# Performance work log

Hardware: AMD Instinct MI355X
Metric: run time of the kernel (lower is better)

Reference implementation:

```python
import jax, jax.numpy as jnp
import numpy as np

# irreps_in = irreps_out = 64x0e + 32x1o
MUL0, MUL1 = 64, 32          # multiplicities of 0e scalars and 1o vectors
DIM_IN = MUL0 + MUL1 * 3     # 160
N_NODES = 50000
IU0, IV0 = np.triu_indices(MUL0, k=1)   # 2016 scalar u<v pairs
IU1, IV1 = np.triu_indices(MUL1, k=1)   # 496 vector u<v pairs
# e3nn path normalization (component / element):
#   i_out=0 (0e): num_elements sum = 2016 + 64 + 496 + 32 = 2608, dim(0e)=1
#   i_out=1 (1o): num_elements = 32*64 = 2048, dim(1o)=3
C0 = float(np.sqrt(1.0 / 2608.0))
C1 = float(np.sqrt(3.0 / 2048.0))
INV_SQRT3 = float(1.0 / np.sqrt(3.0))   # w3j(1,0,1) and w3j(1,1,0) CG factor


def setup_inputs() -> dict:
    key = jax.random.key(0)
    ks = jax.random.split(key, 7)
    node_feats = jax.random.normal(ks[0], (N_NODES, DIM_IN), jnp.float32)
    node_messages = jax.random.normal(ks[1], (N_NODES, DIM_IN), jnp.float32)
    W1 = jax.random.normal(ks[2], (len(IU0), MUL0), jnp.float32)  # (0e,0e)->0e u<vw
    W2 = jax.random.normal(ks[3], (MUL0, MUL0), jnp.float32)      # (0e,0e)->0e uuw
    W3 = jax.random.normal(ks[4], (MUL1, MUL0, MUL1), jnp.float32)  # (1o,0e)->1o uvw
    W4 = jax.random.normal(ks[5], (len(IU1), MUL0), jnp.float32)  # (1o,1o)->0e u<vw
    W5 = jax.random.normal(ks[6], (MUL1, MUL0), jnp.float32)      # (1o,1o)->0e uuw
    return {"node_feats": node_feats, "node_messages": node_messages,
            "W1": W1, "W2": W2, "W3": W3, "W4": W4, "W5": W5}


def _tensor_square(x, W1, W2, W3, W4, W5):
    x0 = x[:, :MUL0]                        # [N, 64] scalars (0e)
    x1 = x[:, MUL0:].reshape(-1, MUL1, 3)   # [N, 32, 3] vectors (1o)
    # (0e x 0e) -> 0e
    pair0 = x0[:, IU0] * x0[:, IV0]         # [N, 2016]
    sq0 = x0 * x0                           # [N, 64]
    # (1o x 1o) -> 0e via dot products (w3j(1,1,0) = delta/sqrt3)
    d = jnp.einsum('nui,nvi->nuv', x1, x1)  # [N, 32, 32]
    pair1 = d[:, IU1, IV1] * INV_SQRT3      # [N, 496]
    diag1 = jnp.einsum('nui,nui->nu', x1, x1) * INV_SQRT3  # [N, 32]
    out0 = C0 * (pair0 @ W1 + sq0 @ W2 + pair1 @ W4 + diag1 @ W5)  # [N, 64]
    # (1o x 0e) -> 1o fully connected uvw (w3j(1,0,1) = eye/sqrt3)
    out1 = (C1 * INV_SQRT3) * jnp.einsum('nui,nv,uvw->nwi', x1, x0, W3)  # [N,32,3]
    return jnp.concatenate([out0, out1.reshape(-1, MUL1 * 3)], axis=1)


def reference(node_feats, node_messages, W1, W2, W3, W4, W5):
    x = node_feats + node_messages
    return _tensor_square(x, W1, W2, W3, W4, W5)
```

## Files before the change

### kernel.cpp

```cpp
#include <hip/hip_runtime.h>

typedef unsigned short u16;
typedef unsigned int u32;

#define N_NODES 50000
#define NB      64

#define BG_OFF  0
#define BT_OFF  262144
#define BH_OFF  327680

#define ASTR   72
#define AHSTR  40
#define XTSTR  68

typedef __attribute__((ext_vector_type(8))) short short8;
typedef __attribute__((ext_vector_type(4))) float f32x4;
union U4S8 { uint4 u; short8 s; };

__device__ __forceinline__ u16 f2bf(float f) {
    u32 u = __float_as_uint(f);
    return (u16)((u + 0x7fffu + ((u >> 16) & 1u)) >> 16);
}

__global__ __launch_bounds__(256)
void pack_kernel(const float* __restrict__ W1, const float* __restrict__ W2,
                 const float* __restrict__ W3, const float* __restrict__ W4,
                 const float* __restrict__ W5, u16* __restrict__ ws) {
    const float INV_SQRT3 = 0.57735026918962576f;
    int T = blockIdx.x * 256 + threadIdx.x;
    float val;
    if (T < BT_OFF) {
        int slot = T;
        int ntile = slot >> 10, rem = slot & 1023;
        int ks = rem >> 9, rem2 = rem & 511;
        int lane = rem2 >> 3, jj = rem2 & 7;
        int v = ks * 32 + (lane >> 4) * 8 + jj;
        int j = ntile * 16 + (lane & 15);
        int u = j >> 6, w = j & 63;
        if (v == u) val = W2[v * 64 + w];
        else {
            int a = min(u, v), b = max(u, v);
            int p = a * (127 - a) / 2 + (b - a - 1);
            val = 0.5f * W1[p * 64 + w];
        }
    } else if (T < BH_OFF) {
        int slot = T - BT_OFF;
        int ntile = slot >> 10, rem = slot & 1023;
        int ks = rem >> 9, rem2 = rem & 511;
        int lane = rem2 >> 3, jj = rem2 & 7;
        int v = ks * 32 + (lane >> 4) * 8 + jj;
        int j = ntile * 16 + (lane & 15);
        int u = j >> 5, w = j & 31;
        val = W3[(u * 64 + v) * 32 + w];
    } else {
        int slot = T - BH_OFF;
        int ntile = slot >> 9, rem = slot & 511;
        int lane = rem >> 3, jj = rem & 7;
        int v = (lane >> 4) * 8 + jj;
        int j = ntile * 16 + (lane & 15);
        int u = j >> 6, w = j & 63;
        if (v == u) val = W5[v * 64 + w] * INV_SQRT3;
        else {
            int a = min(u, v), b = max(u, v);
            int p = a * (63 - a) / 2 + (b - a - 1);
            val = W4[p * 64 + w] * (0.5f * INV_SQRT3);
        }
    }
    ws[T] = f2bf(val);
}

__global__ __launch_bounds__(256)
void node_block_kernel(const float* __restrict__ feats, const float* __restrict__ msgs,
                       const u16* __restrict__ ws, float* __restrict__ out) {
    __shared__ u16  A_S[64 * ASTR];
    __shared__ u16  A_H[192 * AHSTR];
    __shared__ float x0T[64 * XTSTR];
    __shared__ float x1T[96 * XTSTR];

    const int tid = threadIdx.x;
    const int node0 = blockIdx.x * NB;

    for (int k = 0; k < 5; ++k) {
        int chunk = tid + k * 256;
        int idx = chunk * 8;
        int n = (u32)idx / 160u;
        int d = idx - n * 160;
        int g = node0 * 160 + idx;
        float v[8];
        if (g + 8 <= N_NODES * 160) {
            float4 fa0 = *(const float4*)(feats + g);
            float4 fa1 = *(const float4*)(feats + g + 4);
            float4 fb0 = *(const float4*)(msgs + g);
            float4 fb1 = *(const float4*)(msgs + g + 4);
            v[0]=fa0.x+fb0.x; v[1]=fa0.y+fb0.y; v[2]=fa0.z+fb0.z; v[3]=fa0.w+fb0.w;
            v[4]=fa1.x+fb1.x; v[5]=fa1.y+fb1.y; v[6]=fa1.z+fb1.z; v[7]=fa1.w+fb1.w;
        } else {
            #pragma unroll
            for (int j = 0; j < 8; ++j) v[j] = 0.f;
        }
        if (d < 64) {
            uint4 pk;
            pk.x = ((u32)f2bf(v[1]) << 16) | f2bf(v[0]);
            pk.y = ((u32)f2bf(v[3]) << 16) | f2bf(v[2]);
            pk.z = ((u32)f2bf(v[5]) << 16) | f2bf(v[4]);
            pk.w = ((u32)f2bf(v[7]) << 16) | f2bf(v[6]);
            *(uint4*)&A_S[n * ASTR + d] = pk;
            #pragma unroll
            for (int j = 0; j < 8; ++j) x0T[(d + j) * XTSTR + n] = v[j];
        } else {
            #pragma unroll
            for (int j = 0; j < 8; ++j) {
                int dd = d + j - 64;
                int u = (u32)dd / 3u, i = dd - u * 3;
                A_H[(i * 64 + n) * AHSTR + u] = f2bf(v[j]);
                x1T[(u * 3 + i) * XTSTR + n] = v[j];
            }
        }
    }
    __syncthreads();

    const int wave = tid >> 6, lane = tid & 63, quad = lane >> 4, l15 = lane & 15;
    const int wq = wave;
    const f32x4 z4 = {0.f, 0.f, 0.f, 0.f};

    f32x4 o0[4];
    #pragma unroll
    for (int mt = 0; mt < 4; ++mt) o0[mt] = z4;

    {
        short8 aS[4][2];
        #pragma unroll
        for (int mt = 0; mt < 4; ++mt)
            #pragma unroll
            for (int ks = 0; ks < 2; ++ks) {
                U4S8 t; t.u = *(const uint4*)&A_S[(mt * 16 + l15) * ASTR + ks * 32 + quad * 8];
                aS[mt][ks] = t.s;
            }
        const u16* bp = ws + BG_OFF + (u32)wq * 1024 + lane * 8;
        U4S8 b0c, b1c, b0n, b1n;
        b0c.u = *(const uint4*)(bp);
        b1c.u = *(const uint4*)(bp + 512);
        #pragma unroll 1
        for (int u = 0; u < 64; ++u) {
            if (u < 63) {
                b0n.u = *(const uint4*)(bp + 4096);
                b1n.u = *(const uint4*)(bp + 4096 + 512);
            } else { b0n = b0c; b1n = b1c; }
            bp += 4096;
            f32x4 acc[4];
            #pragma unroll
            for (int mt = 0; mt < 4; ++mt) acc[mt] = z4;
            #pragma unroll
            for (int mt = 0; mt < 4; ++mt)
                acc[mt] = __builtin_amdgcn_mfma_f32_16x16x32_bf16(aS[mt][0], b0c.s, acc[mt], 0, 0, 0);
            #pragma unroll
            for (int mt = 0; mt < 4; ++mt)
                acc[mt] = __builtin_amdgcn_mfma_f32_16x16x32_bf16(aS[mt][1], b1c.s, acc[mt], 0, 0, 0);
            #pragma unroll
            for (int mt = 0; mt < 4; ++mt) {
                f32x4 xq = *(const f32x4*)&x0T[u * XTSTR + mt * 16 + quad * 4];
                o0[mt] += xq * acc[mt];
            }
            b0c = b0n; b1c = b1n;
        }
    }

    #pragma unroll 1
    for (int i = 0; i < 3; ++i) {
        short8 aH[4];
        #pragma unroll
        for (int m = 0; m < 4; ++m) {
            U4S8 t; t.u = *(const uint4*)&A_H[((i * 4 + m) * 16 + l15) * AHSTR + quad * 8];
            aH[m] = t.s;
        }
        const u16* bp = ws + BH_OFF + (u32)wq * 512 + lane * 8;
        U4S8 bc, bn;
        bc.u = *(const uint4*)(bp);
        #pragma unroll 1
        for (int u = 0; u < 32; ++u) {
            if (u < 31) bn.u = *(const uint4*)(bp + 2048); else bn = bc;
            bp += 2048;
            f32x4 acc[4];
            #pragma unroll
            for (int m = 0; m < 4; ++m) acc[m] = z4;
            #pragma unroll
            for (int m = 0; m < 4; ++m)
                acc[m] = __builtin_amdgcn_mfma_f32_16x16x32_bf16(aH[m], bc.s, acc[m], 0, 0, 0);
            #pragma unroll
            for (int m = 0; m < 4; ++m) {
                f32x4 xq = *(const f32x4*)&x1T[(u * 3 + i) * XTSTR + m * 16 + quad * 4];
                o0[m] += xq * acc[m];
            }
            bc = bn;
        }
    }

    {
        const float C0v = 0.019581512f;
        #pragma unroll
        for (int mt = 0; mt < 4; ++mt)
            #pragma unroll
            for (int rr = 0; rr < 4; ++rr) {
                int node = node0 + mt * 16 + quad * 4 + rr;
                if (node < N_NODES)
                    out[node * 160 + wq * 16 + l15] = C0v * o0[mt][rr];
            }
    }

    {
        const int mh = wave >> 1, wh = wave & 1;
        short8 aT[2][2];
        #pragma unroll
        for (int m = 0; m < 2; ++m)
            #pragma unroll
            for (int ks = 0; ks < 2; ++ks) {
                U4S8 t; t.u = *(const uint4*)&A_S[((mh * 2 + m) * 16 + l15) * ASTR + ks * 32 + quad * 8];
                aT[m][ks] = t.s;
            }
        f32x4 o1[3][2];
        #pragma unroll
        for (int i = 0; i < 3; ++i)
            #pragma unroll
            for (int m = 0; m < 2; ++m) o1[i][m] = z4;

        const u16* bp = ws + BT_OFF + (u32)wh * 1024 + lane * 8;
        U4S8 b0c, b1c, b0n, b1n;
        b0c.u = *(const uint4*)(bp);
        b1c.u = *(const uint4*)(bp + 512);
        #pragma unroll 1
        for (int u = 0; u < 32; ++u) {
            if (u < 31) {
                b0n.u = *(const uint4*)(bp + 2048);
                b1n.u = *(const uint4*)(bp + 2048 + 512);
            } else { b0n = b0c; b1n = b1c; }
            bp += 2048;
            f32x4 acc[2];
            #pragma unroll
            for (int m = 0; m < 2; ++m) acc[m] = z4;
            #pragma unroll
            for (int m = 0; m < 2; ++m)
                acc[m] = __builtin_amdgcn_mfma_f32_16x16x32_bf16(aT[m][0], b0c.s, acc[m], 0, 0, 0);
            #pragma unroll
            for (int m = 0; m < 2; ++m)
                acc[m] = __builtin_amdgcn_mfma_f32_16x16x32_bf16(aT[m][1], b1c.s, acc[m], 0, 0, 0);
            #pragma unroll
            for (int i = 0; i < 3; ++i)
                #pragma unroll
                for (int m = 0; m < 2; ++m) {
                    f32x4 xq = *(const f32x4*)&x1T[(u * 3 + i) * XTSTR + (mh * 2 + m) * 16 + quad * 4];
                    o1[i][m] += xq * acc[m];
                }
            b0c = b0n; b1c = b1n;
        }
        const float S1 = 0.022097087f;
        #pragma unroll
        for (int i = 0; i < 3; ++i)
            #pragma unroll
            for (int m = 0; m < 2; ++m)
                #pragma unroll
                for (int rr = 0; rr < 4; ++rr) {
                    int node = node0 + (mh * 2 + m) * 16 + quad * 4 + rr;
                    if (node < N_NODES)
                        out[node * 160 + 64 + (wh * 16 + l15) * 3 + i] = S1 * o1[i][m][rr];
                }
    }
}

extern "C" void kernel_launch(void* const* d_in, const int* in_sizes, int n_in,
                              void* d_out, int out_size, void* d_ws, size_t ws_size,
                              hipStream_t stream) {
    const float* feats = (const float*)d_in[0];
    const float* msgs  = (const float*)d_in[1];
    const float* W1    = (const float*)d_in[2];
    const float* W2    = (const float*)d_in[3];
    const float* W3    = (const float*)d_in[4];
    const float* W4    = (const float*)d_in[5];
    const float* W5    = (const float*)d_in[6];
    float* out = (float*)d_out;
    u16* ws = (u16*)d_ws;

    hipLaunchKernelGGL(pack_kernel, dim3(393216 / 256), dim3(256), 0, stream,
                       W1, W2, W3, W4, W5, ws);
    hipLaunchKernelGGL(node_block_kernel, dim3((N_NODES + NB - 1) / NB), dim3(256), 0, stream,
                       feats, msgs, ws, out);
}
```

Baseline: 205.4 us.

## Shrink LDS with bf16 transposed features, reorder weight packing, deepen B prefetch

```diff
diff --git a/kernel.cpp b/kernel.cpp
--- a/kernel.cpp
+++ b/kernel.cpp
@@ -1,4 +1,5 @@
 #include <hip/hip_runtime.h>
+#include <math.h>
 
 typedef unsigned short u16;
 typedef unsigned int u32;
@@ -22,6 +23,34 @@
     u32 u = __float_as_uint(f);
     return (u16)((u + 0x7fffu + ((u >> 16) & 1u)) >> 16);
 }
+__device__ __forceinline__ f32x4 bf4(uint2 q) {
+    f32x4 r;
+    r[0] = __uint_as_float(q.x << 16);
+    r[1] = __uint_as_float(q.x & 0xffff0000u);
+    r[2] = __uint_as_float(q.y << 16);
+    r[3] = __uint_as_float(q.y & 0xffff0000u);
+    return r;
+}
+
+__device__ __forceinline__ int gslot(int u, int v, int w) {
+    int j = u * 64 + w;
+    return (j >> 4) * 1024 + (v >> 5) * 512 + (((v >> 3) & 3) * 16 + (j & 15)) * 8 + (v & 7);
+}
+__device__ __forceinline__ int tslot(int u, int v, int w) {
+    int j = u * 32 + w;
+    return (j >> 4) * 1024 + (v >> 5) * 512 + (((v >> 3) & 3) * 16 + (j & 15)) * 8 + (v & 7);
+}
+__device__ __forceinline__ int hslot(int u, int v, int w) {
+    int j = u * 64 + w;
+    return (j >> 4) * 512 + (((v >> 3) & 3) * 16 + (j & 15)) * 8 + (v & 7);
+}
+
+#define PA (2016 * 64)
+#define PB (64 * 64)
+#define PC (2048 * 32)
+#define PD (496 * 64)
+#define PE (32 * 64)
+#define PTOT (PA + PB + PC + PD + PE)
 
 __global__ __launch_bounds__(256)
 void pack_kernel(const float* __restrict__ W1, const float* __restrict__ W2,
@@ -29,54 +58,50 @@
                  const float* __restrict__ W5, u16* __restrict__ ws) {
     const float INV_SQRT3 = 0.57735026918962576f;
     int T = blockIdx.x * 256 + threadIdx.x;
-    float val;
-    if (T < BT_OFF) {
-        int slot = T;
-        int ntile = slot >> 10, rem = slot & 1023;
-        int ks = rem >> 9, rem2 = rem & 511;
-        int lane = rem2 >> 3, jj = rem2 & 7;
-        int v = ks * 32 + (lane >> 4) * 8 + jj;
-        int j = ntile * 16 + (lane & 15);
-        int u = j >> 6, w = j & 63;
-        if (v == u) val = W2[v * 64 + w];
-        else {
-            int a = min(u, v), b = max(u, v);
-            int p = a * (127 - a) / 2 + (b - a - 1);
-            val = 0.5f * W1[p * 64 + w];
-        }
-    } else if (T < BH_OFF) {
-        int slot = T - BT_OFF;
-        int ntile = slot >> 10, rem = slot & 1023;
-        int ks = rem >> 9, rem2 = rem & 511;
-        int lane = rem2 >> 3, jj = rem2 & 7;
-        int v = ks * 32 + (lane >> 4) * 8 + jj;
-        int j = ntile * 16 + (lane & 15);
-        int u = j >> 5, w = j & 31;
-        val = W3[(u * 64 + v) * 32 + w];
-    } else {
-        int slot = T - BH_OFF;
-        int ntile = slot >> 9, rem = slot & 511;
-        int lane = rem >> 3, jj = rem & 7;
-        int v = (lane >> 4) * 8 + jj;
-        int j = ntile * 16 + (lane & 15);
-        int u = j >> 6, w = j & 63;
-        if (v == u) val = W5[v * 64 + w] * INV_SQRT3;
-        else {
-            int a = min(u, v), b = max(u, v);
-            int p = a * (63 - a) / 2 + (b - a - 1);
-            val = W4[p * 64 + w] * (0.5f * INV_SQRT3);
-        }
-    }
-    ws[T] = f2bf(val);
-}
-
-__global__ __launch_bounds__(256)
+    if (T < PA) {
+        int p = T >> 6, w = T & 63;
+        u16 bv = f2bf(0.5f * W1[T]);
+        int a = (int)((127.0f - sqrtf(16129.0f - 8.0f * (float)p)) * 0.5f);
+        a = max(0, min(a, 62));
+        while (a > 0 && p < a * (127 - a) / 2) --a;
+        while (p >= (a + 1) * (126 - a) / 2) ++a;
+        int b = a + 1 + (p - a * (127 - a) / 2);
+        ws[BG_OFF + gslot(b, a, w)] = bv;
+        ws[BG_OFF + gslot(a, b, w)] = bv;
+    } else if (T < PA + PB) {
+        int t = T - PA;
+        int v = t >> 6, w = t & 63;
+        ws[BG_OFF + gslot(v, v, w)] = f2bf(W2[t]);
+    } else if (T < PA + PB + PC) {
+        int t = T - PA - PB;
+        int k = t >> 5, w = t & 31;
+        int u = k >> 6, v = k & 63;
+        ws[BT_OFF + tslot(u, v, w)] = f2bf(W3[t]);
+    } else if (T < PA + PB + PC + PD) {
+        int t = T - PA - PB - PC;
+        int p = t >> 6, w = t & 63;
+        u16 bv = f2bf(0.5f * INV_SQRT3 * W4[t]);
+        int a = (int)((63.0f - sqrtf(3969.0f - 8.0f * (float)p)) * 0.5f);
+        a = max(0, min(a, 30));
+        while (a > 0 && p < a * (63 - a) / 2) --a;
+        while (p >= (a + 1) * (62 - a) / 2) ++a;
+        int b = a + 1 + (p - a * (63 - a) / 2);
+        ws[BH_OFF + hslot(b, a, w)] = bv;
+        ws[BH_OFF + hslot(a, b, w)] = bv;
+    } else if (T < PTOT) {
+        int t = T - PA - PB - PC - PD;
+        int v = t >> 6, w = t & 63;
+        ws[BH_OFF + hslot(v, v, w)] = f2bf(INV_SQRT3 * W5[t]);
+    }
+}
+
+__global__ __launch_bounds__(256, 3)
 void node_block_kernel(const float* __restrict__ feats, const float* __restrict__ msgs,
                        const u16* __restrict__ ws, float* __restrict__ out) {
-    __shared__ u16  A_S[64 * ASTR];
-    __shared__ u16  A_H[192 * AHSTR];
-    __shared__ float x0T[64 * XTSTR];
-    __shared__ float x1T[96 * XTSTR];
+    __shared__ u16 A_S[64 * ASTR];
+    __shared__ u16 A_H[192 * AHSTR];
+    __shared__ u16 x0T[64 * XTSTR];
+    __shared__ u16 x1T[96 * XTSTR];
 
     const int tid = threadIdx.x;
     const int node0 = blockIdx.x * NB;
@@ -99,22 +124,25 @@
             #pragma unroll
             for (int j = 0; j < 8; ++j) v[j] = 0.f;
         }
+        u16 bv[8];
+        #pragma unroll
+        for (int j = 0; j < 8; ++j) bv[j] = f2bf(v[j]);
         if (d < 64) {
             uint4 pk;
-            pk.x = ((u32)f2bf(v[1]) << 16) | f2bf(v[0]);
-            pk.y = ((u32)f2bf(v[3]) << 16) | f2bf(v[2]);
-            pk.z = ((u32)f2bf(v[5]) << 16) | f2bf(v[4]);
-            pk.w = ((u32)f2bf(v[7]) << 16) | f2bf(v[6]);
+            pk.x = ((u32)bv[1] << 16) | bv[0];
+            pk.y = ((u32)bv[3] << 16) | bv[2];
+            pk.z = ((u32)bv[5] << 16) | bv[4];
+            pk.w = ((u32)bv[7] << 16) | bv[6];
             *(uint4*)&A_S[n * ASTR + d] = pk;
             #pragma unroll
-            for (int j = 0; j < 8; ++j) x0T[(d + j) * XTSTR + n] = v[j];
+            for (int j = 0; j < 8; ++j) x0T[(d + j) * XTSTR + n] = bv[j];
         } else {
             #pragma unroll
             for (int j = 0; j < 8; ++j) {
                 int dd = d + j - 64;
                 int u = (u32)dd / 3u, i = dd - u * 3;
-                A_H[(i * 64 + n) * AHSTR + u] = f2bf(v[j]);
-                x1T[(u * 3 + i) * XTSTR + n] = v[j];
+                A_H[(i * 64 + n) * AHSTR + u] = bv[j];
+                x1T[(u * 3 + i) * XTSTR + n] = bv[j];
             }
         }
     }
@@ -138,31 +166,33 @@
                 aS[mt][ks] = t.s;
             }
         const u16* bp = ws + BG_OFF + (u32)wq * 1024 + lane * 8;
-        U4S8 b0c, b1c, b0n, b1n;
-        b0c.u = *(const uint4*)(bp);
-        b1c.u = *(const uint4*)(bp + 512);
-        #pragma unroll 1
+        U4S8 b0[2], b1[2];
+        b0[0].u = *(const uint4*)(bp);
+        b1[0].u = *(const uint4*)(bp + 512);
+        b0[1].u = *(const uint4*)(bp + 4096);
+        b1[1].u = *(const uint4*)(bp + 4096 + 512);
+        #pragma unroll 2
         for (int u = 0; u < 64; ++u) {
-            if (u < 63) {
-                b0n.u = *(const uint4*)(bp + 4096);
-                b1n.u = *(const uint4*)(bp + 4096 + 512);
-            } else { b0n = b0c; b1n = b1c; }
-            bp += 4096;
+            const int c = u & 1;
+            short8 B0 = b0[c].s, B1 = b1[c].s;
+            if (u < 62) {
+                b0[c].u = *(const uint4*)(bp + (u + 2) * 4096);
+                b1[c].u = *(const uint4*)(bp + (u + 2) * 4096 + 512);
+            }
             f32x4 acc[4];
             #pragma unroll
             for (int mt = 0; mt < 4; ++mt) acc[mt] = z4;
             #pragma unroll
             for (int mt = 0; mt < 4; ++mt)
-                acc[mt] = __builtin_amdgcn_mfma_f32_16x16x32_bf16(aS[mt][0], b0c.s, acc[mt], 0, 0, 0);
+                acc[mt] = __builtin_amdgcn_mfma_f32_16x16x32_bf16(aS[mt][0], B0, acc[mt], 0, 0, 0);
             #pragma unroll
             for (int mt = 0; mt < 4; ++mt)
-                acc[mt] = __builtin_amdgcn_mfma_f32_16x16x32_bf16(aS[mt][1], b1c.s, acc[mt], 0, 0, 0);
+                acc[mt] = __builtin_amdgcn_mfma_f32_16x16x32_bf16(aS[mt][1], B1, acc[mt], 0, 0, 0);
             #pragma unroll
             for (int mt = 0; mt < 4; ++mt) {
-                f32x4 xq = *(const f32x4*)&x0T[u * XTSTR + mt * 16 + quad * 4];
+                f32x4 xq = bf4(*(const uint2*)&x0T[u * XTSTR + mt * 16 + quad * 4]);
                 o0[mt] += xq * acc[mt];
             }
-            b0c = b0n; b1c = b1n;
         }
     }
 
@@ -189,7 +219,7 @@
                 acc[m] = __builtin_amdgcn_mfma_f32_16x16x32_bf16(aH[m], bc.s, acc[m], 0, 0, 0);
             #pragma unroll
             for (int m = 0; m < 4; ++m) {
-                f32x4 xq = *(const f32x4*)&x1T[(u * 3 + i) * XTSTR + m * 16 + quad * 4];
+                f32x4 xq = bf4(*(const uint2*)&x1T[(u * 3 + i) * XTSTR + m * 16 + quad * 4]);
                 o0[m] += xq * acc[m];
             }
             bc = bn;
@@ -225,33 +255,35 @@
             for (int m = 0; m < 2; ++m) o1[i][m] = z4;
 
         const u16* bp = ws + BT_OFF + (u32)wh * 1024 + lane * 8;
-        U4S8 b0c, b1c, b0n, b1n;
-        b0c.u = *(const uint4*)(bp);
-        b1c.u = *(const uint4*)(bp + 512);
-        #pragma unroll 1
+        U4S8 b0[2], b1[2];
+        b0[0].u = *(const uint4*)(bp);
+        b1[0].u = *(const uint4*)(bp + 512);
+        b0[1].u = *(const uint4*)(bp + 2048);
+        b1[1].u = *(const uint4*)(bp + 2048 + 512);
+        #pragma unroll 2
         for (int u = 0; u < 32; ++u) {
-            if (u < 31) {
-                b0n.u = *(const uint4*)(bp + 2048);
-                b1n.u = *(const uint4*)(bp + 2048 + 512);
-            } else { b0n = b0c; b1n = b1c; }
-            bp += 2048;
+            const int c = u & 1;
+            short8 B0 = b0[c].s, B1 = b1[c].s;
+            if (u < 30) {
+                b0[c].u = *(const uint4*)(bp + (u + 2) * 2048);
+                b1[c].u = *(const uint4*)(bp + (u + 2) * 2048 + 512);
+            }
             f32x4 acc[2];
             #pragma unroll
             for (int m = 0; m < 2; ++m) acc[m] = z4;
             #pragma unroll
             for (int m = 0; m < 2; ++m)
-                acc[m] = __builtin_amdgcn_mfma_f32_16x16x32_bf16(aT[m][0], b0c.s, acc[m], 0, 0, 0);
+                acc[m] = __builtin_amdgcn_mfma_f32_16x16x32_bf16(aT[m][0], B0, acc[m], 0, 0, 0);
             #pragma unroll
             for (int m = 0; m < 2; ++m)
-                acc[m] = __builtin_amdgcn_mfma_f32_16x16x32_bf16(aT[m][1], b1c.s, acc[m], 0, 0, 0);
+                acc[m] = __builtin_amdgcn_mfma_f32_16x16x32_bf16(aT[m][1], B1, acc[m], 0, 0, 0);
             #pragma unroll
             for (int i = 0; i < 3; ++i)
                 #pragma unroll
                 for (int m = 0; m < 2; ++m) {
-                    f32x4 xq = *(const f32x4*)&x1T[(u * 3 + i) * XTSTR + (mh * 2 + m) * 16 + quad * 4];
+                    f32x4 xq = bf4(*(const uint2*)&x1T[(u * 3 + i) * XTSTR + (mh * 2 + m) * 16 + quad * 4]);
                     o1[i][m] += xq * acc[m];
                 }
-            b0c = b0n; b1c = b1n;
         }
         const float S1 = 0.022097087f;
         #pragma unroll
@@ -280,7 +312,7 @@
     float* out = (float*)d_out;
     u16* ws = (u16*)d_ws;
 
-    hipLaunchKernelGGL(pack_kernel, dim3(393216 / 256), dim3(256), 0, stream,
+    hipLaunchKernelGGL(pack_kernel, dim3((PTOT + 255) / 256), dim3(256), 0, stream,
                        W1, W2, W3, W4, W5, ws);
     hipLaunchKernelGGL(node_block_kernel, dim3((N_NODES + NB - 1) / NB), dim3(256), 0, stream,
                        feats, msgs, ws, out);
```

After: 204.3 us. Within noise of the previous version (-0.5%).
